# Kernel tuning notes

Hardware: AMD Instinct MI355X
Metric: run time of the kernel (lower is better)

The kernel has to match this reference:

```python
import jax, jax.numpy as jnp
import numpy as np

N_EMBD = 1024
H_DIM = 1024
NB = 16          # blocks resolved by _find_dynamic_num_blocks for all projections
N_MEM = 128
N_FORG = H_DIM - N_MEM
RANK = 64
LOG_DT_INIT = -2.0
EPS = 1.1920929e-07  # torch fp32 finfo eps used by F.rms_norm


def rms_norm(x):
    return x * jax.lax.rsqrt(jnp.mean(jnp.square(x), axis=-1, keepdims=True) + EPS)


def silu(x):
    return x * jax.nn.sigmoid(x)


def blockdiag(x, w):
    # x: [..., nb*bi], w: [nb, bo, bi] -> [..., nb*bo]
    nb, bo, bi = w.shape
    xs = x.reshape(*x.shape[:-1], nb, bi)
    y = jnp.einsum('...ni,noi->...no', xs, w)
    return y.reshape(*x.shape[:-1], nb * bo)


def causal_scan(drive, a):
    # drive: [B,T,D] float32, a: [D] per-channel decay; causal conv with kernel a^t via FFT
    B, T, D = drive.shape
    steps = jnp.arange(T, dtype=jnp.float32)
    kernel = jnp.exp(jnp.log(jnp.maximum(a, 1e-6))[:, None] * steps[None, :])  # [D,T]
    n_fft = 1 << int(2 * T - 1).bit_length()
    df = jnp.fft.rfft(drive.astype(jnp.float32).transpose(0, 2, 1), n=n_fft, axis=-1)
    kf = jnp.fft.rfft(kernel, n=n_fft, axis=-1)
    y = jnp.fft.irfft(df * kf[None], n=n_fft, axis=-1)[..., :T]
    return y.transpose(0, 2, 1).astype(drive.dtype)


def geom_gain(a, K):
    one_minus = 1.0 - a
    safe = jnp.maximum(one_minus, 1e-8)
    return jnp.where(jnp.abs(one_minus) < 1e-6,
                     jnp.full_like(a, float(K)),
                     (1.0 - a ** K) / safe)


def setup_inputs() -> dict:
    key = jax.random.key(0)
    ks = jax.random.split(key, 10)
    s = 0.02
    bi_e, bo_h = N_EMBD // NB, H_DIM // NB
    bi_p = (2 * N_EMBD + H_DIM) // NB
    bo_e = N_EMBD // NB
    return {
        'x': jax.random.normal(ks[0], (4, 4096, N_EMBD), dtype=jnp.float32),
        'active_k': 4,
        'b_seq_w': jax.random.normal(ks[1], (NB, bo_h, bi_e), jnp.float32) * s,
        'b_depth_w': jax.random.normal(ks[2], (NB, bo_h, bi_e), jnp.float32) * s,
        'w_post_w': jax.random.normal(ks[3], (NB, bo_h, bi_p), jnp.float32) * s,
        'w_local_w': jax.random.normal(ks[4], (NB, bo_e, H_DIM // NB), jnp.float32) * s,
        'lr_A': jax.random.normal(ks[5], (N_EMBD, RANK), jnp.float32) * s,
        'lr_B': jax.random.normal(ks[6], (RANK, H_DIM), jnp.float32) * s,
        'log_A_seq': jnp.zeros((H_DIM,), jnp.float32),
        'log_dt_seq': jnp.full((H_DIM,), LOG_DT_INIT, jnp.float32),
        'log_A_depth': jnp.zeros((N_FORG,), jnp.float32),
        'log_dt_depth': jnp.full((N_FORG,), LOG_DT_INIT, jnp.float32),
    }


def reference(x, active_k, b_seq_w, b_depth_w, w_post_w, w_local_w, lr_A, lr_B,
              log_A_seq, log_dt_seq, log_A_depth, log_dt_depth):
    K = int(active_k)
    e = rms_norm(x)
    shifted_e = jnp.pad(e[:, :-1], ((0, 0), (1, 0), (0, 0)))
    a_seq = jnp.exp(-jnp.exp(log_A_seq) * jnp.exp(log_dt_seq))
    h_seq = causal_scan(silu(blockdiag(e, b_seq_w)), a_seq)
    a_forg = jnp.exp(-jnp.exp(log_A_depth) * jnp.exp(log_dt_depth))
    a_depth = jnp.concatenate([jnp.ones((N_MEM,), a_forg.dtype), a_forg], axis=0)
    gain = geom_gain(a_depth, K).astype(x.dtype)
    h_depth = gain * silu(blockdiag(e, b_depth_w))
    h = h_seq + h_depth
    r = silu(blockdiag(jnp.concatenate([rms_norm(h), e, shifted_e], axis=-1), w_post_w))
    out = x + blockdiag(r, w_local_w) + (r @ lr_B.T) @ lr_A.T
    return out
```

## Files before the change

kernel.cpp:

```cpp
#include <hip/hip_runtime.h>

#define B_ 4
#define T_ 4096
#define D_ 1024
#define R_ (B_*T_)
#define CHUNK_ 64
#define NCH_ (T_/CHUNK_)
#define EPS_ 1.1920929e-07f

typedef unsigned short ushort_t;
typedef __attribute__((ext_vector_type(8))) short short8;
typedef __attribute__((ext_vector_type(4))) float f32x4;

__device__ __forceinline__ float silu_f(float v){ return v / (1.0f + __expf(-v)); }

__device__ __forceinline__ ushort_t f2bf(float f){
    unsigned u = __float_as_uint(f);
    unsigned r = u + 0x7fffu + ((u>>16)&1u);
    return (ushort_t)(r>>16);
}
__device__ __forceinline__ float bf2f(ushort_t s){ return __uint_as_float(((unsigned)s)<<16); }

__device__ __forceinline__ f32x4 mfma16(short8 a, short8 b, f32x4 c){
    return __builtin_amdgcn_mfma_f32_16x16x32_bf16(a, b, c, 0, 0, 0);
}

__global__ void prep_k(const float* __restrict__ s0, const float* __restrict__ s1,
                       const float* __restrict__ s2, const float* __restrict__ s3,
                       const float* __restrict__ s4, const float* __restrict__ s5,
                       ushort_t* __restrict__ d0, ushort_t* __restrict__ d1,
                       ushort_t* __restrict__ d2, ushort_t* __restrict__ d3,
                       ushort_t* __restrict__ d4, ushort_t* __restrict__ d5,
                       const float* __restrict__ logA_seq, const float* __restrict__ logdt_seq,
                       const float* __restrict__ logA_dep, const float* __restrict__ logdt_dep,
                       const int* __restrict__ active_k,
                       float* __restrict__ aseq, float* __restrict__ apowC, float* __restrict__ gain){
    int i = blockIdx.x*256 + threadIdx.x;
    if      (i < 65536)   d0[i] = f2bf(s0[i]);
    else if (i < 131072)  d1[i-65536] = f2bf(s1[i-65536]);
    else if (i < 327680)  d2[i-131072] = f2bf(s2[i-131072]);
    else if (i < 393216)  d3[i-327680] = f2bf(s3[i-327680]);
    else if (i < 458752)  d4[i-393216] = f2bf(s4[i-393216]);
    else if (i < 524288)  d5[i-458752] = f2bf(s5[i-458752]);
    else if (i < 524288 + D_){
        int d = i - 524288;
        float K = (float)(*active_k);
        float a = expf(-expf(logA_seq[d]) * expf(logdt_seq[d]));
        a = fmaxf(a, 1e-6f);
        aseq[d] = a;
        apowC[d] = powf(a, (float)CHUNK_);
        float g;
        if (d < 128) {
            g = K;
        } else {
            float ad = expf(-expf(logA_dep[d-128]) * expf(logdt_dep[d-128]));
            float om = 1.0f - ad;
            if (fabsf(om) < 1e-6f) g = K;
            else g = (1.0f - powf(ad, K)) / fmaxf(om, 1e-8f);
        }
        gain[d] = g;
    }
}

__global__ __launch_bounds__(256) void rmsbf_k(const float* __restrict__ x, ushort_t* __restrict__ e){
    int row = blockIdx.x;
    int tid = threadIdx.x;
    float4 v = ((const float4*)(x + (size_t)row*D_))[tid];
    float ss = v.x*v.x + v.y*v.y + v.z*v.z + v.w*v.w;
    for (int off=32; off; off>>=1) ss += __shfl_down(ss, off, 64);
    __shared__ float red[4];
    if ((tid&63)==0) red[tid>>6] = ss;
    __syncthreads();
    float tot = red[0]+red[1]+red[2]+red[3];
    float scale = 1.0f / sqrtf(tot*(1.0f/D_) + EPS_);
    ushort4 o;
    o.x = f2bf(v.x*scale); o.y = f2bf(v.y*scale); o.z = f2bf(v.z*scale); o.w = f2bf(v.w*scale);
    ((ushort4*)(e + (size_t)row*D_))[tid] = o;
}

__global__ __launch_bounds__(256) void bd2s_k(const ushort_t* __restrict__ e,
        const ushort_t* __restrict__ wseq, const ushort_t* __restrict__ wdep,
        const float* __restrict__ gain, const float* __restrict__ aseq,
        ushort_t* __restrict__ hloc, ushort_t* __restrict__ hdep, float* __restrict__ carry){
    __shared__ __align__(16) ushort_t sd[4][64][72];
    __shared__ __align__(16) ushort_t sh[4][16][72];
    int wave = threadIdx.x>>6, lane = threadIdx.x&63;
    int m = lane&15, quad = lane>>4;
    int orow = lane>>2, oq = lane&3;
    int n = blockIdx.y;
    int chunk0 = blockIdx.x*256 + wave*64;

    short8 bs[2][4], bd[2][4];
    #pragma unroll
    for (int s=0;s<2;++s)
        #pragma unroll
        for (int c=0;c<4;++c){
            bs[s][c] = *(const short8*)(wseq + n*4096 + (c*16+m)*64 + s*32 + quad*8);
            bd[s][c] = *(const short8*)(wdep + n*4096 + (c*16+m)*64 + s*32 + quad*8);
        }
    float g[4];
    #pragma unroll
    for (int c=0;c<4;++c) g[c] = gain[n*64 + c*16 + m];

    #pragma unroll
    for (int t=0;t<4;++t){
        int r0 = chunk0 + t*16;
        const ushort_t* ab = e + (size_t)(r0+m)*D_ + n*64 + quad*8;
        short8 a0 = *(const short8*)ab;
        short8 a1 = *(const short8*)(ab + 32);
        f32x4 accs[4], accd[4];
        #pragma unroll
        for (int c=0;c<4;++c){
            accs[c]=(f32x4)0.f; accd[c]=(f32x4)0.f;
            accs[c]=mfma16(a0, bs[0][c], accs[c]);
            accd[c]=mfma16(a0, bd[0][c], accd[c]);
            accs[c]=mfma16(a1, bs[1][c], accs[c]);
            accd[c]=mfma16(a1, bd[1][c], accd[c]);
        }
        #pragma unroll
        for (int c=0;c<4;++c)
            #pragma unroll
            for (int r=0;r<4;++r){
                sd[wave][t*16+quad*4+r][c*16+m] = f2bf(silu_f(accs[c][r]));
                sh[wave][quad*4+r][c*16+m]      = f2bf(g[c]*silu_f(accd[c][r]));
            }
        ushort_t* hb = hdep + (size_t)(r0+orow)*D_ + n*64;
        #pragma unroll
        for (int it=0;it<2;++it)
            *(short8*)(hb + (it*4+oq)*8) = *(const short8*)&sh[wave][orow][(it*4+oq)*8];
    }
    float a = aseq[n*64 + lane];
    float hh = 0.f;
    #pragma unroll 8
    for (int s=0;s<64;++s){
        hh = fmaf(a, hh, bf2f(sd[wave][s][lane]));
        sd[wave][s][lane] = f2bf(hh);
    }
    carry[(size_t)(chunk0>>6)*D_ + n*64 + lane] = hh;
    #pragma unroll
    for (int t=0;t<4;++t){
        ushort_t* db = hloc + (size_t)(chunk0 + t*16 + orow)*D_ + n*64;
        #pragma unroll
        for (int it=0;it<2;++it)
            *(short8*)(db + (it*4+oq)*8) = *(const short8*)&sd[wave][t*16+orow][(it*4+oq)*8];
    }
}

__global__ __launch_bounds__(256) void scan2_k(float* __restrict__ carry, const float* __restrict__ apowC){
    int tid = blockIdx.x*256 + threadIdx.x;
    int d = tid & (D_-1);
    int b = tid >> 10;
    float aC = apowC[d];
    float pref = 0.f;
    for (int c=0;c<NCH_;++c){
        size_t idx = (size_t)(b*NCH_+c)*D_ + d;
        float s = carry[idx];
        carry[idx] = pref;
        pref = fmaf(aC, pref, s);
    }
}

__global__ __launch_bounds__(256) void scan3_k(const ushort_t* __restrict__ hloc,
                                               const ushort_t* __restrict__ hdep,
                                               const float* __restrict__ aseq,
                                               const float* __restrict__ carry,
                                               ushort_t* __restrict__ h){
    int tid = blockIdx.x*256 + threadIdx.x;
    int d  = tid & (D_-1);
    int bc = tid >> 10;
    int c  = bc & (NCH_-1);
    int b  = bc >> 6;
    float a = aseq[d];
    float P = carry[(size_t)bc*D_ + d];
    size_t base = ((size_t)(b*T_ + c*CHUNK_))*D_ + d;
    float apow = a;
    #pragma unroll 4
    for (int s=0; s<CHUNK_; ++s){
        size_t idx = base + (size_t)s*D_;
        h[idx] = f2bf(bf2f(hloc[idx]) + P*apow + bf2f(hdep[idx]));
        apow *= a;
    }
}

__global__ __launch_bounds__(128) void hn_k(const ushort_t* __restrict__ h, ushort_t* __restrict__ hn){
    int row = blockIdx.x;
    int tid = threadIdx.x;
    short8 v = *(const short8*)(h + (size_t)row*D_ + tid*8);
    float f[8];
    float ss = 0.f;
    #pragma unroll
    for (int j=0;j<8;++j){ f[j] = bf2f((ushort_t)v[j]); ss += f[j]*f[j]; }
    for (int off=32; off; off>>=1) ss += __shfl_down(ss, off, 64);
    __shared__ float red[2];
    if ((tid&63)==0) red[tid>>6] = ss;
    __syncthreads();
    float scale = rsqrtf((red[0]+red[1])*(1.0f/D_) + EPS_);
    short8 o;
    #pragma unroll
    for (int j=0;j<8;++j) o[j] = (short)f2bf(f[j]*scale);
    *(short8*)(hn + (size_t)row*D_ + tid*8) = o;
}

__global__ __launch_bounds__(256) void post_k(const ushort_t* __restrict__ hn,
                                              const ushort_t* __restrict__ e,
                                              const ushort_t* __restrict__ wpost, ushort_t* __restrict__ rout){
    __shared__ __align__(16) ushort_t st[4][16][72];
    int wave = threadIdx.x>>6, lane = threadIdx.x&63;
    int m = lane&15, quad = lane>>4;
    int orow = lane>>2, oq = lane&3;
    int n = blockIdx.y;

    short8 bw[6][4];
    #pragma unroll
    for (int s=0;s<6;++s)
        #pragma unroll
        for (int c=0;c<4;++c)
            bw[s][c] = *(const short8*)(wpost + n*(64*192) + (c*16+m)*192 + s*32 + quad*8);

    #pragma unroll
    for (int t=0;t<2;++t){
        int r0 = blockIdx.x*128 + wave*32 + t*16;
        int row = r0 + m;
        bool zrow = ((row & (T_-1)) == 0);
        short8 af[6];
        #pragma unroll
        for (int s=0;s<6;++s){
            int g0 = n*192 + s*32;
            if (g0 < 1024){
                af[s] = *(const short8*)(hn + (size_t)row*D_ + g0 + quad*8);
            } else if (g0 < 2048){
                af[s] = *(const short8*)(e + (size_t)row*D_ + (g0-1024) + quad*8);
            } else {
                if (zrow) af[s] = short8{0,0,0,0,0,0,0,0};
                else      af[s] = *(const short8*)(e + (size_t)(row-1)*D_ + (g0-2048) + quad*8);
            }
        }
        f32x4 acc[4];
        #pragma unroll
        for (int c=0;c<4;++c) acc[c]=(f32x4)0.f;
        #pragma unroll
        for (int s=0;s<6;++s)
            #pragma unroll
            for (int c=0;c<4;++c)
                acc[c] = mfma16(af[s], bw[s][c], acc[c]);
        #pragma unroll
        for (int c=0;c<4;++c)
            #pragma unroll
            for (int r=0;r<4;++r)
                st[wave][quad*4+r][c*16+m] = f2bf(silu_f(acc[c][r]));
        ushort_t* db = rout + (size_t)(r0+orow)*D_ + n*64;
        #pragma unroll
        for (int it=0;it<2;++it)
            *(short8*)(db + (it*4+oq)*8) = *(const short8*)&st[wave][orow][(it*4+oq)*8];
    }
}

__global__ __launch_bounds__(256) void rlow_k(const ushort_t* __restrict__ r, const ushort_t* __restrict__ lrB,
                                              ushort_t* __restrict__ rlow){
    __shared__ __align__(16) float sacc[4][16][68];
    int wave = threadIdx.x>>6, lane = threadIdx.x&63;
    int m = lane&15, quad = lane>>4;
    int r0 = blockIdx.x*16;
    f32x4 acc[4];
    #pragma unroll
    for (int c=0;c<4;++c) acc[c]=(f32x4)0.f;
    const ushort_t* ab = r + (size_t)(r0+m)*D_ + wave*256 + quad*8;
    #pragma unroll
    for (int s=0;s<8;++s){
        short8 a = *(const short8*)(ab + s*32);
        #pragma unroll
        for (int c=0;c<4;++c){
            short8 b = *(const short8*)(lrB + (c*16+m)*1024 + wave*256 + s*32 + quad*8);
            acc[c] = mfma16(a, b, acc[c]);
        }
    }
    #pragma unroll
    for (int c=0;c<4;++c)
        #pragma unroll
        for (int r2=0;r2<4;++r2)
            sacc[wave][quad*4+r2][c*16+m] = acc[c][r2];
    __syncthreads();
    int row  = threadIdx.x>>4;
    int col4 = (threadIdx.x&15)*4;
    float4 v0 = *(const float4*)&sacc[0][row][col4];
    float4 v1 = *(const float4*)&sacc[1][row][col4];
    float4 v2 = *(const float4*)&sacc[2][row][col4];
    float4 v3 = *(const float4*)&sacc[3][row][col4];
    ushort4 o;
    o.x = f2bf(v0.x+v1.x+v2.x+v3.x);
    o.y = f2bf(v0.y+v1.y+v2.y+v3.y);
    o.z = f2bf(v0.z+v1.z+v2.z+v3.z);
    o.w = f2bf(v0.w+v1.w+v2.w+v3.w);
    *(ushort4*)(rlow + (size_t)(r0+row)*64 + col4) = o;
}

__global__ __launch_bounds__(256) void out_k(const float* __restrict__ x, const ushort_t* __restrict__ r,
        const ushort_t* __restrict__ rlow, const ushort_t* __restrict__ wloc, const ushort_t* __restrict__ lrA,
        float* __restrict__ out){
    __shared__ __align__(16) float st[4][16][68];
    int wave = threadIdx.x>>6, lane = threadIdx.x&63;
    int m = lane&15, quad = lane>>4;
    int orow = lane>>2, oq = lane&3;
    int n = blockIdx.y;

    short8 wl[2][4], la[4][2];
    #pragma unroll
    for (int c=0;c<4;++c)
        #pragma unroll
        for (int s=0;s<2;++s){
            wl[s][c] = *(const short8*)(wloc + n*4096 + (c*16+m)*64 + s*32 + quad*8);
            la[c][s] = *(const short8*)(lrA + (size_t)(n*64 + c*16 + m)*64 + s*32 + quad*8);
        }
    #pragma unroll
    for (int t=0;t<2;++t){
        int r0 = blockIdx.x*128 + wave*32 + t*16;
        const float* xb = x + (size_t)(r0+orow)*D_ + n*64;
        float4 xv[4];
        #pragma unroll
        for (int it=0;it<4;++it) xv[it] = *(const float4*)(xb + (it*4+oq)*4);

        const ushort_t* lb = rlow + (size_t)(r0+m)*64 + quad*8;
        short8 al0 = *(const short8*)lb;
        short8 al1 = *(const short8*)(lb + 32);
        const ushort_t* ab = r + (size_t)(r0+m)*D_ + n*64 + quad*8;
        short8 ar0 = *(const short8*)ab;
        short8 ar1 = *(const short8*)(ab + 32);
        f32x4 acc[4];
        #pragma unroll
        for (int c=0;c<4;++c){
            acc[c]=(f32x4)0.f;
            acc[c]=mfma16(al0, la[c][0], acc[c]);
            acc[c]=mfma16(al1, la[c][1], acc[c]);
            acc[c]=mfma16(ar0, wl[0][c], acc[c]);
            acc[c]=mfma16(ar1, wl[1][c], acc[c]);
        }
        #pragma unroll
        for (int c=0;c<4;++c)
            #pragma unroll
            for (int r2=0;r2<4;++r2)
                st[wave][quad*4+r2][c*16+m] = acc[c][r2];
        float* ob = out + (size_t)(r0+orow)*D_ + n*64;
        #pragma unroll
        for (int it=0;it<4;++it){
            float4 v = *(const float4*)&st[wave][orow][(it*4+oq)*4];
            v.x += xv[it].x; v.y += xv[it].y; v.z += xv[it].z; v.w += xv[it].w;
            *(float4*)(ob + (it*4+oq)*4) = v;
        }
    }
}

extern "C" void kernel_launch(void* const* d_in, const int* in_sizes, int n_in,
                              void* d_out, int out_size, void* d_ws, size_t ws_size,
                              hipStream_t stream) {
    const float* x         = (const float*)d_in[0];
    const int*   active_k  = (const int*)  d_in[1];
    const float* b_seq_w   = (const float*)d_in[2];
    const float* b_depth_w = (const float*)d_in[3];
    const float* w_post_w  = (const float*)d_in[4];
    const float* w_local_w = (const float*)d_in[5];
    const float* lr_A      = (const float*)d_in[6];
    const float* lr_B      = (const float*)d_in[7];
    const float* logA_seq  = (const float*)d_in[8];
    const float* logdt_seq = (const float*)d_in[9];
    const float* logA_dep  = (const float*)d_in[10];
    const float* logdt_dep = (const float*)d_in[11];

    float* ws    = (float*)d_ws;
    float* carry = ws;
    float* aseq  = carry + (size_t)B_*NCH_*D_;
    float* apowC = aseq + D_;
    float* gain  = apowC + D_;
    ushort_t* ub       = (ushort_t*)(gain + D_);
    ushort_t* e_bf     = ub;
    ushort_t* hloc_bf  = e_bf + (size_t)R_*D_;
    ushort_t* hdep_bf  = hloc_bf + (size_t)R_*D_;
    ushort_t* h_bf     = hdep_bf + (size_t)R_*D_;
    ushort_t* r_bf     = h_bf + (size_t)R_*D_;
    ushort_t* rlow_bf  = r_bf + (size_t)R_*D_;
    ushort_t* wseq_bf  = rlow_bf + (size_t)R_*64;
    ushort_t* wdep_bf  = wseq_bf + 65536;
    ushort_t* wpost_bf = wdep_bf + 65536;
    ushort_t* wloc_bf  = wpost_bf + 196608;
    ushort_t* lrA_bf   = wloc_bf + 65536;
    ushort_t* lrB_bf   = lrA_bf + 65536;
    ushort_t* hn_bf    = hloc_bf;

    prep_k<<<(524288 + D_ + 255)/256, 256, 0, stream>>>(
        b_seq_w, b_depth_w, w_post_w, w_local_w, lr_A, lr_B,
        wseq_bf, wdep_bf, wpost_bf, wloc_bf, lrA_bf, lrB_bf,
        logA_seq, logdt_seq, logA_dep, logdt_dep, active_k, aseq, apowC, gain);

    rmsbf_k<<<R_, 256, 0, stream>>>(x, e_bf);
    bd2s_k <<<dim3(R_/256, 16), 256, 0, stream>>>(e_bf, wseq_bf, wdep_bf, gain, aseq,
                                                  hloc_bf, hdep_bf, carry);
    scan2_k<<<(B_*D_)/256, 256, 0, stream>>>(carry, apowC);
    scan3_k<<<(B_*NCH_*D_)/256, 256, 0, stream>>>(hloc_bf, hdep_bf, aseq, carry, h_bf);
    hn_k   <<<R_, 128, 0, stream>>>(h_bf, hn_bf);
    post_k <<<dim3(R_/128, 16), 256, 0, stream>>>(hn_bf, e_bf, wpost_bf, r_bf);
    rlow_k <<<R_/16, 256, 0, stream>>>(r_bf, lrB_bf, rlow_bf);
    out_k  <<<dim3(R_/128, 16), 256, 0, stream>>>(x, r_bf, rlow_bf, wloc_bf, lrA_bf, (float*)d_out);
}
```

Before: 308.6 us.

## Fuse depth term into local scan output and apply RMS scale inside post GEMM

After: 285.8 us. -7.4%, faster.

```diff
diff --git a/kernel.cpp b/kernel.cpp
--- a/kernel.cpp
+++ b/kernel.cpp
@@ -81,8 +81,8 @@
 __global__ __launch_bounds__(256) void bd2s_k(const ushort_t* __restrict__ e,
         const ushort_t* __restrict__ wseq, const ushort_t* __restrict__ wdep,
         const float* __restrict__ gain, const float* __restrict__ aseq,
-        ushort_t* __restrict__ hloc, ushort_t* __restrict__ hdep, float* __restrict__ carry){
-    __shared__ __align__(16) ushort_t sd[4][64][72];
+        ushort_t* __restrict__ hsum, float* __restrict__ carry){
+    __shared__ __align__(16) ushort_t sd[4][16][72];
     __shared__ __align__(16) ushort_t sh[4][16][72];
     int wave = threadIdx.x>>6, lane = threadIdx.x&63;
     int m = lane&15, quad = lane>>4;
@@ -101,6 +101,9 @@
     float g[4];
     #pragma unroll
     for (int c=0;c<4;++c) g[c] = gain[n*64 + c*16 + m];
+
+    float a = aseq[n*64 + lane];
+    float hh = 0.f;
 
     #pragma unroll
     for (int t=0;t<4;++t){
@@ -121,29 +124,20 @@
         for (int c=0;c<4;++c)
             #pragma unroll
             for (int r=0;r<4;++r){
-                sd[wave][t*16+quad*4+r][c*16+m] = f2bf(silu_f(accs[c][r]));
-                sh[wave][quad*4+r][c*16+m]      = f2bf(g[c]*silu_f(accd[c][r]));
+                sd[wave][quad*4+r][c*16+m] = f2bf(silu_f(accs[c][r]));
+                sh[wave][quad*4+r][c*16+m] = f2bf(g[c]*silu_f(accd[c][r]));
             }
-        ushort_t* hb = hdep + (size_t)(r0+orow)*D_ + n*64;
+        #pragma unroll
+        for (int s=0;s<16;++s){
+            hh = fmaf(a, hh, bf2f(sd[wave][s][lane]));
+            sd[wave][s][lane] = f2bf(hh + bf2f(sh[wave][s][lane]));
+        }
+        ushort_t* db = hsum + (size_t)(r0+orow)*D_ + n*64;
         #pragma unroll
         for (int it=0;it<2;++it)
-            *(short8*)(hb + (it*4+oq)*8) = *(const short8*)&sh[wave][orow][(it*4+oq)*8];
-    }
-    float a = aseq[n*64 + lane];
-    float hh = 0.f;
-    #pragma unroll 8
-    for (int s=0;s<64;++s){
-        hh = fmaf(a, hh, bf2f(sd[wave][s][lane]));
-        sd[wave][s][lane] = f2bf(hh);
+            *(short8*)(db + (it*4+oq)*8) = *(const short8*)&sd[wave][orow][(it*4+oq)*8];
     }
     carry[(size_t)(chunk0>>6)*D_ + n*64 + lane] = hh;
-    #pragma unroll
-    for (int t=0;t<4;++t){
-        ushort_t* db = hloc + (size_t)(chunk0 + t*16 + orow)*D_ + n*64;
-        #pragma unroll
-        for (int it=0;it<2;++it)
-            *(short8*)(db + (it*4+oq)*8) = *(const short8*)&sd[wave][t*16+orow][(it*4+oq)*8];
-    }
 }
 
 __global__ __launch_bounds__(256) void scan2_k(float* __restrict__ carry, const float* __restrict__ apowC){
@@ -160,8 +154,7 @@
     }
 }
 
-__global__ __launch_bounds__(256) void scan3_k(const ushort_t* __restrict__ hloc,
-                                               const ushort_t* __restrict__ hdep,
+__global__ __launch_bounds__(256) void scan3_k(const ushort_t* __restrict__ hsum,
                                                const float* __restrict__ aseq,
                                                const float* __restrict__ carry,
                                                ushort_t* __restrict__ h){
@@ -177,31 +170,26 @@
     #pragma unroll 4
     for (int s=0; s<CHUNK_; ++s){
         size_t idx = base + (size_t)s*D_;
-        h[idx] = f2bf(bf2f(hloc[idx]) + P*apow + bf2f(hdep[idx]));
+        h[idx] = f2bf(bf2f(hsum[idx]) + P*apow);
         apow *= a;
     }
 }
 
-__global__ __launch_bounds__(128) void hn_k(const ushort_t* __restrict__ h, ushort_t* __restrict__ hn){
-    int row = blockIdx.x;
-    int tid = threadIdx.x;
-    short8 v = *(const short8*)(h + (size_t)row*D_ + tid*8);
-    float f[8];
+__global__ __launch_bounds__(256) void scale_k(const ushort_t* __restrict__ h, float* __restrict__ scale){
+    int wave = threadIdx.x>>6, lane = threadIdx.x&63;
+    int row = blockIdx.x*4 + wave;
+    const ushort_t* hb = h + (size_t)row*D_ + lane*16;
+    short8 v0 = *(const short8*)hb;
+    short8 v1 = *(const short8*)(hb + 8);
     float ss = 0.f;
     #pragma unroll
-    for (int j=0;j<8;++j){ f[j] = bf2f((ushort_t)v[j]); ss += f[j]*f[j]; }
+    for (int j=0;j<8;++j){ float f0 = bf2f((ushort_t)v0[j]); float f1 = bf2f((ushort_t)v1[j]); ss += f0*f0 + f1*f1; }
     for (int off=32; off; off>>=1) ss += __shfl_down(ss, off, 64);
-    __shared__ float red[2];
-    if ((tid&63)==0) red[tid>>6] = ss;
-    __syncthreads();
-    float scale = rsqrtf((red[0]+red[1])*(1.0f/D_) + EPS_);
-    short8 o;
-    #pragma unroll
-    for (int j=0;j<8;++j) o[j] = (short)f2bf(f[j]*scale);
-    *(short8*)(hn + (size_t)row*D_ + tid*8) = o;
-}
-
-__global__ __launch_bounds__(256) void post_k(const ushort_t* __restrict__ hn,
+    if (lane==0) scale[row] = rsqrtf(ss*(1.0f/D_) + EPS_);
+}
+
+__global__ __launch_bounds__(256) void post_k(const ushort_t* __restrict__ h,
+                                              const float* __restrict__ scale,
                                               const ushort_t* __restrict__ e,
                                               const ushort_t* __restrict__ wpost, ushort_t* __restrict__ rout){
     __shared__ __align__(16) ushort_t st[4][16][72];
@@ -209,45 +197,53 @@
     int m = lane&15, quad = lane>>4;
     int orow = lane>>2, oq = lane&3;
     int n = blockIdx.y;
-
-    short8 bw[6][4];
-    #pragma unroll
-    for (int s=0;s<6;++s)
+    int row0 = blockIdx.x*128 + wave*32 + m;
+
+    float scl[2];
+    #pragma unroll
+    for (int t=0;t<2;++t) scl[t] = (n*192 < 1024) ? scale[row0 + t*16] : 0.f;
+
+    f32x4 acc[2][4];
+    #pragma unroll
+    for (int t=0;t<2;++t)
+        #pragma unroll
+        for (int c=0;c<4;++c) acc[t][c]=(f32x4)0.f;
+
+    #pragma unroll 1
+    for (int s=0;s<6;++s){
+        int g0 = n*192 + s*32;
+        short8 bw[4];
         #pragma unroll
         for (int c=0;c<4;++c)
-            bw[s][c] = *(const short8*)(wpost + n*(64*192) + (c*16+m)*192 + s*32 + quad*8);
-
+            bw[c] = *(const short8*)(wpost + n*(64*192) + (c*16+m)*192 + s*32 + quad*8);
+        #pragma unroll
+        for (int t=0;t<2;++t){
+            int row = row0 + t*16;
+            short8 af;
+            if (g0 < 1024){
+                short8 hv = *(const short8*)(h + (size_t)row*D_ + g0 + quad*8);
+                float sc = scl[t];
+                #pragma unroll
+                for (int j=0;j<8;++j) af[j] = (short)f2bf(bf2f((ushort_t)hv[j])*sc);
+            } else if (g0 < 2048){
+                af = *(const short8*)(e + (size_t)row*D_ + (g0-1024) + quad*8);
+            } else {
+                if ((row & (T_-1)) == 0) af = short8{0,0,0,0,0,0,0,0};
+                else af = *(const short8*)(e + (size_t)(row-1)*D_ + (g0-2048) + quad*8);
+            }
+            #pragma unroll
+            for (int c=0;c<4;++c)
+                acc[t][c] = mfma16(af, bw[c], acc[t][c]);
+        }
+    }
     #pragma unroll
     for (int t=0;t<2;++t){
         int r0 = blockIdx.x*128 + wave*32 + t*16;
-        int row = r0 + m;
-        bool zrow = ((row & (T_-1)) == 0);
-        short8 af[6];
-        #pragma unroll
-        for (int s=0;s<6;++s){
-            int g0 = n*192 + s*32;
-            if (g0 < 1024){
-                af[s] = *(const short8*)(hn + (size_t)row*D_ + g0 + quad*8);
-            } else if (g0 < 2048){
-                af[s] = *(const short8*)(e + (size_t)row*D_ + (g0-1024) + quad*8);
-            } else {
-                if (zrow) af[s] = short8{0,0,0,0,0,0,0,0};
-                else      af[s] = *(const short8*)(e + (size_t)(row-1)*D_ + (g0-2048) + quad*8);
-            }
-        }
-        f32x4 acc[4];
-        #pragma unroll
-        for (int c=0;c<4;++c) acc[c]=(f32x4)0.f;
-        #pragma unroll
-        for (int s=0;s<6;++s)
-            #pragma unroll
-            for (int c=0;c<4;++c)
-                acc[c] = mfma16(af[s], bw[s][c], acc[c]);
         #pragma unroll
         for (int c=0;c<4;++c)
             #pragma unroll
             for (int r=0;r<4;++r)
-                st[wave][quad*4+r][c*16+m] = f2bf(silu_f(acc[c][r]));
+                st[wave][quad*4+r][c*16+m] = f2bf(silu_f(acc[t][c][r]));
         ushort_t* db = rout + (size_t)(r0+orow)*D_ + n*64;
         #pragma unroll
         for (int it=0;it<2;++it)
@@ -370,11 +366,11 @@
     float* aseq  = carry + (size_t)B_*NCH_*D_;
     float* apowC = aseq + D_;
     float* gain  = apowC + D_;
-    ushort_t* ub       = (ushort_t*)(gain + D_);
+    float* scale = gain + D_;
+    ushort_t* ub       = (ushort_t*)(scale + R_);
     ushort_t* e_bf     = ub;
-    ushort_t* hloc_bf  = e_bf + (size_t)R_*D_;
-    ushort_t* hdep_bf  = hloc_bf + (size_t)R_*D_;
-    ushort_t* h_bf     = hdep_bf + (size_t)R_*D_;
+    ushort_t* hsum_bf  = e_bf + (size_t)R_*D_;
+    ushort_t* h_bf     = hsum_bf + (size_t)R_*D_;
     ushort_t* r_bf     = h_bf + (size_t)R_*D_;
     ushort_t* rlow_bf  = r_bf + (size_t)R_*D_;
     ushort_t* wseq_bf  = rlow_bf + (size_t)R_*64;
@@ -383,7 +379,6 @@
     ushort_t* wloc_bf  = wpost_bf + 196608;
     ushort_t* lrA_bf   = wloc_bf + 65536;
     ushort_t* lrB_bf   = lrA_bf + 65536;
-    ushort_t* hn_bf    = hloc_bf;
 
     prep_k<<<(524288 + D_ + 255)/256, 256, 0, stream>>>(
         b_seq_w, b_depth_w, w_post_w, w_local_w, lr_A, lr_B,
@@ -392,11 +387,11 @@
 
     rmsbf_k<<<R_, 256, 0, stream>>>(x, e_bf);
     bd2s_k <<<dim3(R_/256, 16), 256, 0, stream>>>(e_bf, wseq_bf, wdep_bf, gain, aseq,
-                                                  hloc_bf, hdep_bf, carry);
+                                                  hsum_bf, carry);
     scan2_k<<<(B_*D_)/256, 256, 0, stream>>>(carry, apowC);
-    scan3_k<<<(B_*NCH_*D_)/256, 256, 0, stream>>>(hloc_bf, hdep_bf, aseq, carry, h_bf);
-    hn_k   <<<R_, 128, 0, stream>>>(h_bf, hn_bf);
-    post_k <<<dim3(R_/128, 16), 256, 0, stream>>>(hn_bf, e_bf, wpost_bf, r_bf);
+    scan3_k<<<(B_*NCH_*D_)/256, 256, 0, stream>>>(hsum_bf, aseq, carry, h_bf);
+    scale_k<<<R_/4, 256, 0, stream>>>(h_bf, scale);
+    post_k <<<dim3(R_/128, 16), 256, 0, stream>>>(h_bf, scale, e_bf, wpost_bf, r_bf);
     rlow_k <<<R_/16, 256, 0, stream>>>(r_bf, lrB_bf, rlow_bf);
     out_k  <<<dim3(R_/128, 16), 256, 0, stream>>>(x, r_bf, rlow_bf, wloc_bf, lrA_bf, (float*)d_out);
 }
```
